# Optimization experiments

Hardware: AMD Instinct MI355X
Metric: run time of the kernel (lower is better)

## Reference

```python
import jax, jax.numpy as jnp
import numpy as np

RADII = (1.5, 3.0)   # max radii per dilated ring
KS = (32, 64)        # neighbors per ring
OP_C = 64            # per-operator output channels
OUT_C = 256          # agg conv output channels


def setup_inputs() -> dict:
    key = jax.random.key(0)
    k = jax.random.split(key, 8)
    B, N, M, D, C = 4, 8192, 2048, 3, 64
    positions = jax.random.normal(k[0], (B, N, D), dtype=jnp.float32)
    features = jax.random.normal(k[1], (B, N, C), dtype=jnp.float32)
    centers = jax.random.normal(k[2], (B, M, D), dtype=jnp.float32)
    # squared distances in [0, 9) so both rings [1,2.25) and [2.25,9) are hit
    distances = jax.random.uniform(k[3], (B, M, N), dtype=jnp.float32) * 9.0
    W_op0 = jax.random.normal(k[4], (D + C, OP_C), dtype=jnp.float32) * 0.05
    b_op0 = jnp.zeros((OP_C,), dtype=jnp.float32)
    W_op1 = jax.random.normal(k[5], (D + C, OP_C), dtype=jnp.float32) * 0.05
    b_op1 = jnp.zeros((OP_C,), dtype=jnp.float32)
    W_agg = jax.random.normal(k[6], (2 * OP_C, OUT_C), dtype=jnp.float32) * 0.05
    b_agg = jnp.zeros((OUT_C,), dtype=jnp.float32)
    return dict(positions=positions, features=features, centers=centers,
                distances=distances, W_op0=W_op0, b_op0=b_op0,
                W_op1=W_op1, b_op1=b_op1, W_agg=W_agg, b_agg=b_agg)


def reference(positions, features, centers, distances,
              W_op0, b_op0, W_op1, b_op1, W_agg, b_agg):
    B, N, D = positions.shape
    M = centers.shape[1]
    arangeN = jnp.arange(N)
    bidx = jnp.arange(B)[:, None, None]
    min_radius = -1.0  # faithful to source: min_radius**2 == 1 in ring 0
    fs = []
    for max_radius, kk, (W, b) in zip(RADII, KS, ((W_op0, b_op0), (W_op1, b_op1))):
        excluded = (distances >= max_radius ** 2) | (distances < min_radius ** 2)
        idx = jnp.where(excluded, N, arangeN[None, None, :])   # (B,M,N)
        idx = jnp.sort(idx, axis=-1)[:, :, :kk]                # (B,M,k)
        mask = idx != N
        safe = jnp.where(mask, idx, 0)
        pos_g = positions[bidx, safe]                          # (B,M,k,D)
        feat_g = features[bidx, safe]                          # (B,M,k,C)
        rel = pos_g - centers[:, :, None, :]                   # (B,M,k,D)
        h = jax.nn.relu(jnp.concatenate([rel, feat_g], axis=-1) @ W + b)
        h = jnp.where(mask[..., None], h, 0.0)                 # invalid -> zero row
        fs.append(jnp.max(h, axis=2))                          # (B,M,OP_C)
        min_radius = max_radius
    x = jnp.concatenate(fs, axis=-1)                           # (B,M,2*OP_C)
    return jax.nn.relu(x @ W_agg + b_agg)                      # (B,M,OUT_C)
```

## Files before the change

### kernel.cpp

```cpp
#include <hip/hip_runtime.h>
#include <stdint.h>

#define BB 4
#define NN 8192
#define MM 2048
#define CC 64
#define OPC 64
#define OUTC 256
#define K0 32
#define K1 64
#define NCH 9
#define CPW 4

typedef short bf16x8 __attribute__((ext_vector_type(8)));
typedef float f32x4  __attribute__((ext_vector_type(4)));

__device__ __forceinline__ short f2bf(float f) {
    uint32_t u = __float_as_uint(f);
    u += 0x7FFFu + ((u >> 16) & 1u);
    return (short)(u >> 16);
}

__device__ __forceinline__ uint32_t cvt_pk_bf16(float a, float b) {
    uint32_t r;
    asm("v_cvt_pk_bf16_f32 %0, %1, %2" : "=v"(r) : "v"(a), "v"(b));
    return r;
}

template <int ROWS>
__device__ __forceinline__ void stage_row(short (*sA)[ROWS][8], int row,
                                          const float* __restrict__ pos,
                                          const float* __restrict__ feat,
                                          float cx, float cy, float cz) {
    const float4* fp4 = (const float4*)feat;
    float4 q[16];
#pragma unroll
    for (int t = 0; t < 16; ++t) q[t] = fp4[t];
#pragma unroll
    for (int c = 0; c < 8; ++c) {
        float4 a = q[2 * c], b = q[2 * c + 1];
        uint4 v;
        v.x = cvt_pk_bf16(a.x, a.y);
        v.y = cvt_pk_bf16(a.z, a.w);
        v.z = cvt_pk_bf16(b.x, b.y);
        v.w = cvt_pk_bf16(b.z, b.w);
        *(uint4*)&sA[c][row][0] = v;
    }
    float rx = pos[0] - cx, ry = pos[1] - cy, rz = pos[2] - cz;
    uint4 vr;
    vr.x = cvt_pk_bf16(rx, ry);
    vr.y = cvt_pk_bf16(rz, 0.0f);
    vr.z = 0u; vr.w = 0u;
    *(uint4*)&sA[8][row][0] = vr;
}

__global__ __launch_bounds__(256, 2) void op_kernel(
    const float* __restrict__ positions, const float* __restrict__ features,
    const float* __restrict__ centers,   const float* __restrict__ distances,
    const float* __restrict__ W0, const float* __restrict__ b0,
    const float* __restrict__ W1, const float* __restrict__ b1,
    const float* __restrict__ Wagg, const float* __restrict__ bagg,
    float* __restrict__ out)
{
    __shared__ __align__(16) short sA1[4][NCH][K1][8];
    __shared__ __align__(16) short sA0[4][NCH][K0][8];
    __shared__ float s_x[4][CPW][128];
    __shared__ int s_idx0[4][K0];
    __shared__ int s_idx1[4][K1];

    const int w    = threadIdx.x >> 6;
    const int lane = threadIdx.x & 63;
    const int quad = lane >> 4;
    const int l15  = lane & 15;
    const int gw   = blockIdx.x * 4 + w;

    bf16x8 bfr0[3][4], bfr1[3][4];
#pragma unroll
    for (int kc = 0; kc < 3; ++kc) {
#pragma unroll
        for (int nt = 0; nt < 4; ++nt) {
            const int n = nt * 16 + l15;
            bf16x8 v0, v1;
#pragma unroll
            for (int j = 0; j < 8; ++j) {
                int k = kc * 32 + quad * 8 + j;
                float a0 = 0.f, a1 = 0.f;
                if (k < 64)      { a0 = W0[(3 + k) * OPC + n];  a1 = W1[(3 + k) * OPC + n]; }
                else if (k < 67) { a0 = W0[(k - 64) * OPC + n]; a1 = W1[(k - 64) * OPC + n]; }
                v0[j] = f2bf(a0); v1[j] = f2bf(a1);
            }
            bfr0[kc][nt] = v0; bfr1[kc][nt] = v1;
        }
    }
    float bias0v[4], bias1v[4];
#pragma unroll
    for (int nt = 0; nt < 4; ++nt) {
        bias0v[nt] = b0[nt * 16 + l15];
        bias1v[nt] = b1[nt * 16 + l15];
    }
    const unsigned long long lt = (1ull << lane) - 1ull;

    for (int i = 0; i < CPW; ++i) {
        const int bm = gw * CPW + i;
        const int b  = bm >> 11;

        const float* drow = distances + (size_t)bm * NN;
        int cnt0 = 0, cnt1 = 0;
        for (int base = 0; base < NN; base += 512) {
            if (cnt0 >= K0 && cnt1 >= K1) break;
            float dv[8];
#pragma unroll
            for (int u = 0; u < 8; ++u) dv[u] = drow[base + u * 64 + lane];
#pragma unroll
            for (int u = 0; u < 8; ++u) {
                float d = dv[u];
                bool p0 = (d >= 1.0f)  && (d < 2.25f);
                bool p1 = (d >= 2.25f) && (d < 9.0f);
                unsigned long long m0 = __ballot(p0);
                unsigned long long m1 = __ballot(p1);
                if (cnt0 < K0) {
                    int pos = cnt0 + __popcll(m0 & lt);
                    if (p0 && pos < K0) s_idx0[w][pos] = base + u * 64 + lane;
                    cnt0 += __popcll(m0);
                }
                if (cnt1 < K1) {
                    int pos = cnt1 + __popcll(m1 & lt);
                    if (p1 && pos < K1) s_idx1[w][pos] = base + u * 64 + lane;
                    cnt1 += __popcll(m1);
                }
            }
        }
        cnt0 = min(cnt0, K0);
        cnt1 = min(cnt1, K1);

        const float cx = centers[(size_t)bm * 3 + 0];
        const float cy = centers[(size_t)bm * 3 + 1];
        const float cz = centers[(size_t)bm * 3 + 2];

        {
            int n1 = (lane < cnt1) ? s_idx1[w][lane] : 0;
            stage_row<K1>(sA1[w], lane,
                          positions + (size_t)((size_t)b * NN + n1) * 3,
                          features  + (size_t)((size_t)b * NN + n1) * CC,
                          cx, cy, cz);
        }
        if (lane < K0) {
            int n0 = (lane < cnt0) ? s_idx0[w][lane] : 0;
            stage_row<K0>(sA0[w], lane,
                          positions + (size_t)((size_t)b * NN + n0) * 3,
                          features  + (size_t)((size_t)b * NN + n0) * CC,
                          cx, cy, cz);
        }

        {
            float cm[4] = {0.f, 0.f, 0.f, 0.f};
#pragma unroll
            for (int mt = 0; mt < 4; ++mt) {
                bf16x8 af[3];
#pragma unroll
                for (int kc = 0; kc < 3; ++kc) {
                    int ch = (kc < 2) ? kc * 4 + quad : 8;
                    af[kc] = *(bf16x8*)&sA1[w][ch][mt * 16 + l15][0];
                }
                f32x4 acc[4];
#pragma unroll
                for (int nt = 0; nt < 4; ++nt)
                    acc[nt] = (f32x4){bias1v[nt], bias1v[nt], bias1v[nt], bias1v[nt]};
#pragma unroll
                for (int kc = 0; kc < 3; ++kc)
#pragma unroll
                    for (int nt = 0; nt < 4; ++nt)
                        acc[nt] = __builtin_amdgcn_mfma_f32_16x16x32_bf16(
                            af[kc], bfr1[kc][nt], acc[nt], 0, 0, 0);
#pragma unroll
                for (int nt = 0; nt < 4; ++nt)
#pragma unroll
                    for (int r = 0; r < 4; ++r) {
                        int m = mt * 16 + quad * 4 + r;
                        float v = (m < cnt1) ? fmaxf(acc[nt][r], 0.f) : 0.f;
                        cm[nt] = fmaxf(cm[nt], v);
                    }
            }
#pragma unroll
            for (int nt = 0; nt < 4; ++nt) {
                cm[nt] = fmaxf(cm[nt], __shfl_xor(cm[nt], 16, 64));
                cm[nt] = fmaxf(cm[nt], __shfl_xor(cm[nt], 32, 64));
            }
            float f = (quad == 0) ? cm[0] : (quad == 1) ? cm[1]
                    : (quad == 2) ? cm[2] : cm[3];
            s_x[w][i][64 + lane] = f;
        }

        {
            float cm[4] = {0.f, 0.f, 0.f, 0.f};
#pragma unroll
            for (int mt = 0; mt < 2; ++mt) {
                bf16x8 af[3];
#pragma unroll
                for (int kc = 0; kc < 3; ++kc) {
                    int ch = (kc < 2) ? kc * 4 + quad : 8;
                    af[kc] = *(bf16x8*)&sA0[w][ch][mt * 16 + l15][0];
                }
                f32x4 acc[4];
#pragma unroll
                for (int nt = 0; nt < 4; ++nt)
                    acc[nt] = (f32x4){bias0v[nt], bias0v[nt], bias0v[nt], bias0v[nt]};
#pragma unroll
                for (int kc = 0; kc < 3; ++kc)
#pragma unroll
                    for (int nt = 0; nt < 4; ++nt)
                        acc[nt] = __builtin_amdgcn_mfma_f32_16x16x32_bf16(
                            af[kc], bfr0[kc][nt], acc[nt], 0, 0, 0);
#pragma unroll
                for (int nt = 0; nt < 4; ++nt)
#pragma unroll
                    for (int r = 0; r < 4; ++r) {
                        int m = mt * 16 + quad * 4 + r;
                        float v = (m < cnt0) ? fmaxf(acc[nt][r], 0.f) : 0.f;
                        cm[nt] = fmaxf(cm[nt], v);
                    }
            }
#pragma unroll
            for (int nt = 0; nt < 4; ++nt) {
                cm[nt] = fmaxf(cm[nt], __shfl_xor(cm[nt], 16, 64));
                cm[nt] = fmaxf(cm[nt], __shfl_xor(cm[nt], 32, 64));
            }
            float f = (quad == 0) ? cm[0] : (quad == 1) ? cm[1]
                    : (quad == 2) ? cm[2] : cm[3];
            s_x[w][i][lane] = f;
        }
    }

    {
        float4 bias4 = ((const float4*)bagg)[lane];
        f32x4 acc[CPW];
#pragma unroll
        for (int i = 0; i < CPW; ++i)
            acc[i] = (f32x4){bias4.x, bias4.y, bias4.z, bias4.w};

#pragma unroll 2
        for (int c4 = 0; c4 < 32; ++c4) {
            float4 xv[CPW];
#pragma unroll
            for (int i = 0; i < CPW; ++i)
                xv[i] = *(const float4*)&s_x[w][i][c4 * 4];
#pragma unroll
            for (int u = 0; u < 4; ++u) {
                const int c = c4 * 4 + u;
                float4 wv = *(const float4*)(Wagg + (size_t)c * OUTC + lane * 4);
#pragma unroll
                for (int i = 0; i < CPW; ++i) {
                    const float xc = (u == 0) ? xv[i].x : (u == 1) ? xv[i].y
                                   : (u == 2) ? xv[i].z : xv[i].w;
                    acc[i][0] = fmaf(xc, wv.x, acc[i][0]);
                    acc[i][1] = fmaf(xc, wv.y, acc[i][1]);
                    acc[i][2] = fmaf(xc, wv.z, acc[i][2]);
                    acc[i][3] = fmaf(xc, wv.w, acc[i][3]);
                }
            }
        }
#pragma unroll
        for (int i = 0; i < CPW; ++i) {
            float4 o = make_float4(fmaxf(acc[i][0], 0.f), fmaxf(acc[i][1], 0.f),
                                   fmaxf(acc[i][2], 0.f), fmaxf(acc[i][3], 0.f));
            *(float4*)(out + (size_t)(gw * CPW + i) * OUTC + lane * 4) = o;
        }
    }
}

extern "C" void kernel_launch(void* const* d_in, const int* in_sizes, int n_in,
                              void* d_out, int out_size, void* d_ws, size_t ws_size,
                              hipStream_t stream) {
    const float* positions = (const float*)d_in[0];
    const float* features  = (const float*)d_in[1];
    const float* centers   = (const float*)d_in[2];
    const float* distances = (const float*)d_in[3];
    const float* W0        = (const float*)d_in[4];
    const float* b0        = (const float*)d_in[5];
    const float* W1        = (const float*)d_in[6];
    const float* b1        = (const float*)d_in[7];
    const float* Wagg      = (const float*)d_in[8];
    const float* bagg      = (const float*)d_in[9];
    float* out = (float*)d_out;
    (void)d_ws; (void)ws_size;

    op_kernel<<<512, 256, 0, stream>>>(positions, features, centers, distances,
                                       W0, b0, W1, b1, Wagg, bagg, out);
}
```

Baseline: 353.4 us.

## Load gathered neighbor features directly into MFMA A-fragments, drop LDS staging

Removes the shared-memory staging buffers for gathered neighbor rows. Each lane now loads its MFMA A-operand slice of the neighbor features and relative position straight from global memory and packs it to bf16 in registers. This cuts LDS writes and reads and frees LDS, which may allow higher occupancy. In exchange, each lane reads smaller strided 32-byte chunks per row instead of whole contiguous rows, and the relative position is recomputed redundantly by all quads.

```diff
diff --git a/kernel.cpp b/kernel.cpp
--- a/kernel.cpp
+++ b/kernel.cpp
@@ -9,7 +9,6 @@
 #define OUTC 256
 #define K0 32
 #define K1 64
-#define NCH 9
 #define CPW 4
 
 typedef short bf16x8 __attribute__((ext_vector_type(8)));
@@ -27,31 +26,13 @@
     return r;
 }
 
-template <int ROWS>
-__device__ __forceinline__ void stage_row(short (*sA)[ROWS][8], int row,
-                                          const float* __restrict__ pos,
-                                          const float* __restrict__ feat,
-                                          float cx, float cy, float cz) {
-    const float4* fp4 = (const float4*)feat;
-    float4 q[16];
-#pragma unroll
-    for (int t = 0; t < 16; ++t) q[t] = fp4[t];
-#pragma unroll
-    for (int c = 0; c < 8; ++c) {
-        float4 a = q[2 * c], b = q[2 * c + 1];
-        uint4 v;
-        v.x = cvt_pk_bf16(a.x, a.y);
-        v.y = cvt_pk_bf16(a.z, a.w);
-        v.z = cvt_pk_bf16(b.x, b.y);
-        v.w = cvt_pk_bf16(b.z, b.w);
-        *(uint4*)&sA[c][row][0] = v;
-    }
-    float rx = pos[0] - cx, ry = pos[1] - cy, rz = pos[2] - cz;
-    uint4 vr;
-    vr.x = cvt_pk_bf16(rx, ry);
-    vr.y = cvt_pk_bf16(rz, 0.0f);
-    vr.z = 0u; vr.w = 0u;
-    *(uint4*)&sA[8][row][0] = vr;
+__device__ __forceinline__ bf16x8 pack8(float4 a, float4 b) {
+    union { uint4 u; bf16x8 v; } r;
+    r.u.x = cvt_pk_bf16(a.x, a.y);
+    r.u.y = cvt_pk_bf16(a.z, a.w);
+    r.u.z = cvt_pk_bf16(b.x, b.y);
+    r.u.w = cvt_pk_bf16(b.z, b.w);
+    return r.v;
 }
 
 __global__ __launch_bounds__(256, 2) void op_kernel(
@@ -62,8 +43,6 @@
     const float* __restrict__ Wagg, const float* __restrict__ bagg,
     float* __restrict__ out)
 {
-    __shared__ __align__(16) short sA1[4][NCH][K1][8];
-    __shared__ __align__(16) short sA0[4][NCH][K0][8];
     __shared__ float s_x[4][CPW][128];
     __shared__ int s_idx0[4][K0];
     __shared__ int s_idx1[4][K1];
@@ -99,6 +78,7 @@
         bias1v[nt] = b1[nt * 16 + l15];
     }
     const unsigned long long lt = (1ull << lane) - 1ull;
+    const bf16x8 zf = {0, 0, 0, 0, 0, 0, 0, 0};
 
     for (int i = 0; i < CPW; ++i) {
         const int bm = gw * CPW + i;
@@ -138,46 +118,43 @@
         const float cz = centers[(size_t)bm * 3 + 2];
 
         {
-            int n1 = (lane < cnt1) ? s_idx1[w][lane] : 0;
-            stage_row<K1>(sA1[w], lane,
-                          positions + (size_t)((size_t)b * NN + n1) * 3,
-                          features  + (size_t)((size_t)b * NN + n1) * CC,
-                          cx, cy, cz);
-        }
-        if (lane < K0) {
-            int n0 = (lane < cnt0) ? s_idx0[w][lane] : 0;
-            stage_row<K0>(sA0[w], lane,
-                          positions + (size_t)((size_t)b * NN + n0) * 3,
-                          features  + (size_t)((size_t)b * NN + n0) * CC,
-                          cx, cy, cz);
-        }
-
-        {
             float cm[4] = {0.f, 0.f, 0.f, 0.f};
 #pragma unroll
             for (int mt = 0; mt < 4; ++mt) {
-                bf16x8 af[3];
-#pragma unroll
-                for (int kc = 0; kc < 3; ++kc) {
-                    int ch = (kc < 2) ? kc * 4 + quad : 8;
-                    af[kc] = *(bf16x8*)&sA1[w][ch][mt * 16 + l15][0];
-                }
+                const int r = mt * 16 + l15;
+                const int n = (r < cnt1) ? s_idx1[w][r] : 0;
+                const float4* fb = (const float4*)(features + (size_t)((size_t)b * NN + n) * CC);
+                float4 a0 = fb[quad * 2],     a1 = fb[quad * 2 + 1];
+                float4 a2 = fb[8 + quad * 2], a3 = fb[8 + quad * 2 + 1];
+                const float* pp = positions + (size_t)((size_t)b * NN + n) * 3;
+                float rx = pp[0] - cx, ry = pp[1] - cy, rz = pp[2] - cz;
+                bf16x8 af0 = pack8(a0, a1);
+                bf16x8 af1 = pack8(a2, a3);
+                union { uint4 u; bf16x8 v; } r2;
+                r2.u.x = cvt_pk_bf16(rx, ry);
+                r2.u.y = cvt_pk_bf16(rz, 0.0f);
+                r2.u.z = 0u; r2.u.w = 0u;
+                bf16x8 af2 = (quad == 0) ? r2.v : zf;
+
                 f32x4 acc[4];
 #pragma unroll
                 for (int nt = 0; nt < 4; ++nt)
                     acc[nt] = (f32x4){bias1v[nt], bias1v[nt], bias1v[nt], bias1v[nt]};
 #pragma unroll
-                for (int kc = 0; kc < 3; ++kc)
-#pragma unroll
-                    for (int nt = 0; nt < 4; ++nt)
-                        acc[nt] = __builtin_amdgcn_mfma_f32_16x16x32_bf16(
-                            af[kc], bfr1[kc][nt], acc[nt], 0, 0, 0);
-#pragma unroll
-                for (int nt = 0; nt < 4; ++nt)
-#pragma unroll
-                    for (int r = 0; r < 4; ++r) {
-                        int m = mt * 16 + quad * 4 + r;
-                        float v = (m < cnt1) ? fmaxf(acc[nt][r], 0.f) : 0.f;
+                for (int nt = 0; nt < 4; ++nt)
+                    acc[nt] = __builtin_amdgcn_mfma_f32_16x16x32_bf16(af0, bfr1[0][nt], acc[nt], 0, 0, 0);
+#pragma unroll
+                for (int nt = 0; nt < 4; ++nt)
+                    acc[nt] = __builtin_amdgcn_mfma_f32_16x16x32_bf16(af1, bfr1[1][nt], acc[nt], 0, 0, 0);
+#pragma unroll
+                for (int nt = 0; nt < 4; ++nt)
+                    acc[nt] = __builtin_amdgcn_mfma_f32_16x16x32_bf16(af2, bfr1[2][nt], acc[nt], 0, 0, 0);
+#pragma unroll
+                for (int nt = 0; nt < 4; ++nt)
+#pragma unroll
+                    for (int rr = 0; rr < 4; ++rr) {
+                        int m = mt * 16 + quad * 4 + rr;
+                        float v = (m < cnt1) ? fmaxf(acc[nt][rr], 0.f) : 0.f;
                         cm[nt] = fmaxf(cm[nt], v);
                     }
             }
@@ -195,28 +172,40 @@
             float cm[4] = {0.f, 0.f, 0.f, 0.f};
 #pragma unroll
             for (int mt = 0; mt < 2; ++mt) {
-                bf16x8 af[3];
-#pragma unroll
-                for (int kc = 0; kc < 3; ++kc) {
-                    int ch = (kc < 2) ? kc * 4 + quad : 8;
-                    af[kc] = *(bf16x8*)&sA0[w][ch][mt * 16 + l15][0];
-                }
+                const int r = mt * 16 + l15;
+                const int n = (r < cnt0) ? s_idx0[w][r] : 0;
+                const float4* fb = (const float4*)(features + (size_t)((size_t)b * NN + n) * CC);
+                float4 a0 = fb[quad * 2],     a1 = fb[quad * 2 + 1];
+                float4 a2 = fb[8 + quad * 2], a3 = fb[8 + quad * 2 + 1];
+                const float* pp = positions + (size_t)((size_t)b * NN + n) * 3;
+                float rx = pp[0] - cx, ry = pp[1] - cy, rz = pp[2] - cz;
+                bf16x8 af0 = pack8(a0, a1);
+                bf16x8 af1 = pack8(a2, a3);
+                union { uint4 u; bf16x8 v; } r2;
+                r2.u.x = cvt_pk_bf16(rx, ry);
+                r2.u.y = cvt_pk_bf16(rz, 0.0f);
+                r2.u.z = 0u; r2.u.w = 0u;
+                bf16x8 af2 = (quad == 0) ? r2.v : zf;
+
                 f32x4 acc[4];
 #pragma unroll
                 for (int nt = 0; nt < 4; ++nt)
                     acc[nt] = (f32x4){bias0v[nt], bias0v[nt], bias0v[nt], bias0v[nt]};
 #pragma unroll
-                for (int kc = 0; kc < 3; ++kc)
-#pragma unroll
-                    for (int nt = 0; nt < 4; ++nt)
-                        acc[nt] = __builtin_amdgcn_mfma_f32_16x16x32_bf16(
-                            af[kc], bfr0[kc][nt], acc[nt], 0, 0, 0);
-#pragma unroll
-                for (int nt = 0; nt < 4; ++nt)
-#pragma unroll
-                    for (int r = 0; r < 4; ++r) {
-                        int m = mt * 16 + quad * 4 + r;
-                        float v = (m < cnt0) ? fmaxf(acc[nt][r], 0.f) : 0.f;
+                for (int nt = 0; nt < 4; ++nt)
+                    acc[nt] = __builtin_amdgcn_mfma_f32_16x16x32_bf16(af0, bfr0[0][nt], acc[nt], 0, 0, 0);
+#pragma unroll
+                for (int nt = 0; nt < 4; ++nt)
+                    acc[nt] = __builtin_amdgcn_mfma_f32_16x16x32_bf16(af1, bfr0[1][nt], acc[nt], 0, 0, 0);
+#pragma unroll
+                for (int nt = 0; nt < 4; ++nt)
+                    acc[nt] = __builtin_amdgcn_mfma_f32_16x16x32_bf16(af2, bfr0[2][nt], acc[nt], 0, 0, 0);
+#pragma unroll
+                for (int nt = 0; nt < 4; ++nt)
+#pragma unroll
+                    for (int rr = 0; rr < 4; ++rr) {
+                        int m = mt * 16 + quad * 4 + rr;
+                        float v = (m < cnt0) ? fmaxf(acc[nt][rr], 0.f) : 0.f;
                         cm[nt] = fmaxf(cm[nt], v);
                     }
             }
```

New measurement: 353.6 us (median of 2 runs). About the same (+0.1%).
